# Performance work log

Hardware: AMD Instinct MI355X
Metric: run time of the kernel (lower is better)

## Reference

```python
import jax, jax.numpy as jnp
import numpy as np

DN = ('NCDHW', 'DHWIO', 'NCDHW')


def _w(key, cin, cout):
    # kernel_size=3 in 3D, Minkowski-style fan-in scaling, no bias
    scale = 1.0 / np.sqrt(cin * 27)
    return jax.random.normal(key, (3, 3, 3, cin, cout), dtype=jnp.float32) * scale


def setup_inputs() -> dict:
    key = jax.random.key(0)
    ks = jax.random.split(key, 7)
    x = jax.random.normal(ks[0], (1, 1024, 4, 4, 4), dtype=jnp.float32)
    chans = [(1024, 512), (512, 256), (256, 128), (128, 64), (64, 32), (32, 1)]
    ws = {f'w{i+1}': _w(ks[i + 1], ci, co) for i, (ci, co) in enumerate(chans)}
    return {'x': x, **ws}


def _ct(x, w, stride):
    # conv-transpose, kernel 3, SAME padding: stride 2 doubles resolution,
    # stride 1 preserves it (dense analog of Minkowski generative transpose conv)
    return jax.lax.conv_transpose(x, w, strides=(stride, stride, stride),
                                  padding='SAME', dimension_numbers=DN)


def reference(x, w1, w2, w3, w4, w5, w6):
    h = jax.nn.relu(_ct(x, w1, 2))   # 1024 -> 512, 4^3 -> 8^3
    h = jax.nn.relu(_ct(h, w2, 1))   # 512 -> 256
    h = jax.nn.relu(_ct(h, w3, 2))   # 256 -> 128, 8^3 -> 16^3
    h = jax.nn.relu(_ct(h, w4, 1))   # 128 -> 64
    h = jax.nn.relu(_ct(h, w5, 2))   # 64 -> 32, 16^3 -> 32^3
    return _ct(h, w6, 1)             # 32 -> 1, no final ReLU
```

## Files before the change

### kernel.cpp

```cpp
#include <hip/hip_runtime.h>

typedef _Float16 half8 __attribute__((ext_vector_type(8)));
typedef _Float16 half4v __attribute__((ext_vector_type(4)));
typedef float floatx4 __attribute__((ext_vector_type(4)));


__global__ __launch_bounds__(256) void pad_x_k(const float* __restrict__ X,
                                               _Float16* __restrict__ P) {
  int idx = blockIdx.x * 256 + threadIdx.x;
  if (idx >= 125 * 1024) return;
  int c = idx & 1023;
  int r = idx >> 10;
  int px = r % 5, py = (r / 5) % 5, pz = r / 25;
  float v = 0.f;
  if (px >= 1 && py >= 1 && pz >= 1)
    v = X[c * 64 + (pz - 1) * 16 + (py - 1) * 4 + (px - 1)];
  P[idx] = (_Float16)v;
}

template <int POS, int COUT, int S2IN, int NSPL, int PS>
__global__ __launch_bounds__(256) void red_k(const float* __restrict__ Pp,
                                             _Float16* __restrict__ P) {
  constexpr int C4 = COUT / 4;
  constexpr size_t U3 =
      S2IN ? (size_t)(POS / 2) * (POS / 2) * (POS / 2) : (size_t)POS * POS * POS;
  int idx = blockIdx.x * 256 + threadIdx.x;
  if (idx >= PS * PS * PS * C4) return;
  const int co = (idx % C4) * 4;
  const int r = idx / C4;
  const int px = r % PS, py = (r / PS) % PS, pz = r / (PS * PS);
  const int ix = px - 1, iy = py - 1, iz = pz - 1;
  float4 s = make_float4(0.f, 0.f, 0.f, 0.f);
  if ((unsigned)ix < (unsigned)POS && (unsigned)iy < (unsigned)POS &&
      (unsigned)iz < (unsigned)POS) {
    int j0, j1;
    size_t upos;
    if (S2IN) {
      const int pf[8] = {0, 8, 12, 16, 18, 22, 24, 26};
      const int tc[8] = {8, 4, 4, 2, 4, 2, 2, 1};
      const int cls = ((iz & 1) << 2) | ((iy & 1) << 1) | (ix & 1);
      j0 = pf[cls] * NSPL;
      j1 = j0 + tc[cls] * NSPL;
      constexpr int U = POS / 2;
      upos = ((size_t)(iz >> 1) * U + (iy >> 1)) * U + (ix >> 1);
    } else {
      j0 = 0;
      j1 = NSPL;
      upos = ((size_t)iz * POS + iy) * POS + ix;
    }
    const float* base = Pp + upos * COUT + co;
    for (int j = j0; j < j1; j++) {
      float4 v = *(const float4*)(base + (size_t)j * U3 * COUT);
      s.x += v.x; s.y += v.y; s.z += v.z; s.w += v.w;
    }
  }
  half4v h;
  h[0] = (_Float16)fmaxf(s.x, 0.f);
  h[1] = (_Float16)fmaxf(s.y, 0.f);
  h[2] = (_Float16)fmaxf(s.z, 0.f);
  h[3] = (_Float16)fmaxf(s.w, 0.f);
  *(half4v*)(P + (size_t)idx * 4) = h;
}

template <int CICHUNK, int CIN, int COUT, int NTILE, int TZ, int SOUTU,
          int PS, int SMODE, int TAPG, int STORE_MODE>
__global__ __launch_bounds__(256) void conv_mfma_k(
    const _Float16* __restrict__ P, const float* __restrict__ W,
    void* __restrict__ Optr) {
  constexpr int M = TZ * 16;
  constexpr bool S2 = (SMODE != 0);
  constexpr int MTZ = SOUTU / TZ;
  constexpr int MTXY = SOUTU / 4;
  constexpr int MT3 = MTZ * MTXY * MTXY;
  constexpr int KB = 32;
  constexpr int KP = 40;
  constexpr int KBI = CICHUNK / KB;
  constexpr int NCI = CIN / CICHUNK;
  constexpr int S = S2 ? 2 * SOUTU : SOUTU;
  constexpr int WM = (M == 128) ? 4 : 2;
  constexpr int NSUB = (WM == 4) ? (NTILE / 16) : (NTILE / 32);
  constexpr int BJ = KB * NTILE / 256;
  constexpr size_t U3 = (size_t)SOUTU * SOUTU * SOUTU;

  __shared__ __align__(16) _Float16 As[M][KP];
  __shared__ __align__(16) _Float16 Bs[NTILE][KP];

  int bx = blockIdx.x;
  int cls = 0, tap0 = 0, cig = blockIdx.z, jspl = 0;
  int p_toz = 0, p_toy = 0, p_tox = 0, p_wtap = 0;
  if (SMODE == 0) {
    const int tg = cig / NCI;
    cig -= tg * NCI;
    tap0 = tg * TAPG;
    jspl = blockIdx.z;
  } else if (SMODE == 1) {
    const int p = bx / MT3;
    bx -= p * MT3;
    jspl = p * NCI + cig;
    cls = (p >= 8) + (p >= 12) + (p >= 16) + (p >= 18) + (p >= 22) +
          (p >= 24) + (p >= 26);
    const int pf = cls == 0 ? 0 : cls == 1 ? 8 : cls == 2 ? 12
                 : cls == 3 ? 16 : cls == 4 ? 18 : cls == 5 ? 22
                 : cls == 6 ? 24 : 26;
    const int tl = p - pf;
    const int lz = (cls >> 2) & 1, ly = (cls >> 1) & 1, lx = cls & 1;
    const int shx = lx ? 0 : 1, shy = ly ? 0 : 1;
    const int iz = tl >> (shx + shy);
    const int rem = tl & ((1 << (shx + shy)) - 1);
    const int iy = rem >> shx;
    const int ix = rem & ((1 << shx) - 1);
    p_toz = lz ? 1 : iz;
    p_toy = ly ? 1 : iy;
    p_tox = lx ? 1 : ix;
    const int wz = lz ? 1 : 2 * iz, wy = ly ? 1 : 2 * iy,
              wx = lx ? 1 : 2 * ix;
    p_wtap = (wz * 3 + wy) * 3 + wx;
  } else {
    cls = bx / MT3;
    bx -= cls * MT3;
  }
  const int clz = (cls >> 2) & 1, cly = (cls >> 1) & 1, clx = cls & 1;

  const int u0z = (bx / (MTXY * MTXY)) * TZ;
  const int u0y = ((bx / MTXY) % MTXY) * 4;
  const int u0x = (bx % MTXY) * 4;
  const int n_base = blockIdx.y * NTILE;

  const int t = threadIdx.x;
  const int lane = t & 63;
  const int wave = t >> 6;

  const int skq = t & 3;
  const int sp = t >> 2;
  const int spx = sp & 3, spy = (sp >> 2) & 3, spz = sp >> 4;
  const int nB = t & (NTILE - 1);
  const int k0B = (t / NTILE) * BJ;
  const int m0w = (WM == 4) ? wave * 32 : (wave >> 1) * 32;
  const int n0w = (WM == 4) ? 0 : (wave & 1) * 32;
  const int fr = lane & 15;
  const int fq = lane >> 4;

  const int cz = S2 ? (clz ? 1 : 2) : 3;
  const int cy = S2 ? (cly ? 1 : 2) : 3;
  const int cx = S2 ? (clx ? 1 : 2) : 3;
  const int shx2 = clx ? 0 : 1, shy2 = cly ? 0 : 1;

  int NIT;
  if (SMODE == 0) NIT = TAPG * KBI;
  else if (SMODE == 1) NIT = KBI;
  else NIT = cz * cy * cx * KBI;

  floatx4 acc[2][NSUB];
#pragma unroll
  for (int i = 0; i < 2; i++)
#pragma unroll
    for (int s = 0; s < NSUB; s++) acc[i][s] = {0.f, 0.f, 0.f, 0.f};

  half8 rA0 = {}, rA1 = {}, nA0 = {}, nA1 = {};
  float rB[BJ] = {}, nBv[BJ] = {};

  auto load_it = [&](int it, half8& A0, half8& A1, float* BW) {
    int tap, kb;
    if (SMODE == 1) { tap = 0; kb = it; }
    else if (KBI == 1) { tap = it; kb = 0; }
    else { tap = it / KBI; kb = it - tap * KBI; }
    int toz, toy, tox, wtap;
    if (SMODE == 1) {
      toz = p_toz; toy = p_toy; tox = p_tox; wtap = p_wtap;
    } else if (SMODE == 0) {
      const int tt = tap0 + tap;
      const int iz = tt / 9;
      const int rem = tt - iz * 9;
      const int iy = rem / 3;
      const int ix = rem - iy * 3;
      toz = iz; toy = iy; tox = ix;
      wtap = tt;
    } else {
      const int iz = tap >> (shx2 + shy2);
      const int rem = tap & ((1 << (shx2 + shy2)) - 1);
      const int iy = rem >> shx2;
      const int ix = rem & ((1 << shx2) - 1);
      toz = clz ? 1 : iz; toy = cly ? 1 : iy; tox = clx ? 1 : ix;
      const int wz = clz ? 1 : 2 * iz, wy = cly ? 1 : 2 * iy,
                wx = clx ? 1 : 2 * ix;
      wtap = (wz * 3 + wy) * 3 + wx;
    }
    const int kof0 = cig * CICHUNK + kb * KB;
    const size_t pb =
        ((size_t)(((u0z + toz + spz) * PS + (u0y + toy + spy)) * PS +
                  (u0x + tox + spx))) * CIN + kof0 + skq * 8;
    A0 = *(const half8*)(P + pb);
    if (M == 128)
      A1 = *(const half8*)(P + pb + (size_t)4 * PS * PS * CIN);
    const float* wb =
        W + ((size_t)wtap * CIN + kof0 + k0B) * COUT + n_base + nB;
#pragma unroll
    for (int j = 0; j < BJ; j++) BW[j] = wb[(size_t)j * COUT];
  };

  load_it(0, rA0, rA1, rB);

  for (int it = 0; it < NIT; ++it) {
    *(half8*)&As[sp][skq * 8] = rA0;
    if (M == 128) *(half8*)&As[sp + 64][skq * 8] = rA1;
    if (BJ == 8) {
      half8 hb;
#pragma unroll
      for (int j = 0; j < 8; j++) hb[j] = (_Float16)rB[j];
      *(half8*)&Bs[nB][k0B] = hb;
    } else {
      half4v hb;
#pragma unroll
      for (int j = 0; j < 4; j++) hb[j] = (_Float16)rB[j];
      *(half4v*)&Bs[nB][k0B] = hb;
    }
    __syncthreads();
    if (it + 1 < NIT) load_it(it + 1, nA0, nA1, nBv);
    half8 a0 = *(const half8*)&As[m0w + fr][fq * 8];
    half8 a1 = *(const half8*)&As[m0w + 16 + fr][fq * 8];
#pragma unroll
    for (int s = 0; s < NSUB; s++) {
      half8 b = *(const half8*)&Bs[n0w + s * 16 + fr][fq * 8];
      acc[0][s] = __builtin_amdgcn_mfma_f32_16x16x32_f16(a0, b, acc[0][s], 0, 0, 0);
      acc[1][s] = __builtin_amdgcn_mfma_f32_16x16x32_f16(a1, b, acc[1][s], 0, 0, 0);
    }
    __syncthreads();
    rA0 = nA0;
    rA1 = nA1;
#pragma unroll
    for (int j = 0; j < BJ; j++) rB[j] = nBv[j];
  }

#pragma unroll
  for (int i = 0; i < 2; i++) {
#pragma unroll
    for (int r = 0; r < 4; r++) {
      const int m = m0w + i * 16 + fq * 4 + r;
      const int mz = m >> 4, my = (m >> 2) & 3, mx = m & 3;
      if (STORE_MODE == 2) {
        const int oz = 2 * (u0z + mz) + clz;
        const int oy = 2 * (u0y + my) + cly;
        const int ox = 2 * (u0x + mx) + clx;
        _Float16* o = (_Float16*)Optr +
            ((size_t)(((oz + 1) * (S + 2) + (oy + 1)) * (S + 2) + (ox + 1))) *
                COUT + n_base + n0w;
#pragma unroll
        for (int s = 0; s < NSUB; s++)
          o[s * 16 + fr] = (_Float16)fmaxf(acc[i][s][r], 0.f);
      } else {
        const size_t pos =
            ((size_t)((u0z + mz) * SOUTU + (u0y + my))) * SOUTU + (u0x + mx);
        float* o = (float*)Optr + ((size_t)jspl * U3 + pos) * COUT + n_base +
                   n0w;
#pragma unroll
        for (int s = 0; s < NSUB; s++) o[s * 16 + fr] = acc[i][s][r];
      }
    }
  }
}

__global__ __launch_bounds__(256) void conv6_k(const _Float16* __restrict__ P,
                                               const float* __restrict__ W6,
                                               float* __restrict__ O) {
  __shared__ __align__(16) float w[864];
  for (int i = threadIdx.x; i < 864; i += 256) w[i] = W6[i];
  __syncthreads();
  int idx = blockIdx.x * 256 + threadIdx.x;
  int x = idx & 31, y = (idx >> 5) & 31, z = idx >> 10;
  float a = 0.f;
  for (int dz = 0; dz < 3; dz++)
    for (int dy = 0; dy < 3; dy++)
      for (int dx = 0; dx < 3; dx++) {
        const _Float16* p =
            P + (size_t)(((z + dz) * 34 + (y + dy)) * 34 + (x + dx)) * 32;
        const float* ww = &w[((dz * 3 + dy) * 3 + dx) * 32];
#pragma unroll
        for (int c = 0; c < 32; c += 8) {
          half8 pv = *(const half8*)&p[c];
#pragma unroll
          for (int u = 0; u < 8; u++) a += (float)pv[u] * ww[c + u];
        }
      }
  O[idx] = a;
}

extern "C" void kernel_launch(void* const* d_in, const int* in_sizes, int n_in,
                              void* d_out, int out_size, void* d_ws,
                              size_t ws_size, hipStream_t stream) {
  const float* x  = (const float*)d_in[0];
  const float* w1 = (const float*)d_in[1];
  const float* w2 = (const float*)d_in[2];
  const float* w3 = (const float*)d_in[3];
  const float* w4 = (const float*)d_in[4];
  const float* w5 = (const float*)d_in[5];
  const float* w6 = (const float*)d_in[6];
  float* out = (float*)d_out;

  float* Q1 = (float*)d_ws;
  float* Q2 = Q1 + 3538944;
  float* Q3 = Q2 + 3145728;
  float* Q4 = Q3 + 3538944;
  _Float16* P1 = (_Float16*)(Q4 + 3145728);
  _Float16* P2 = P1 + 128000;
  _Float16* P3 = P2 + 512000;
  _Float16* P4 = P3 + 186624;
  _Float16* P5 = P4 + 746496;
  _Float16* P6 = P5 + 314432;

  hipMemsetAsync(P6, 0, 1257728 * sizeof(_Float16), stream);

  pad_x_k<<<500, 256, 0, stream>>>(x, P1);
  conv_mfma_k<256, 1024, 512, 64, 4, 4, 5, 1, 0, 3>
      <<<dim3(27, 8, 4), 256, 0, stream>>>(P1, w1, Q1);
  red_k<8, 512, 1, 4, 10><<<500, 256, 0, stream>>>(Q1, P2);
  conv_mfma_k<64, 512, 256, 64, 8, 8, 10, 0, 9, 3>
      <<<dim3(4, 4, 24), 256, 0, stream>>>(P2, w2, Q2);
  red_k<8, 256, 0, 24, 9><<<183, 256, 0, stream>>>(Q2, P3);
  conv_mfma_k<128, 256, 128, 64, 8, 8, 9, 1, 0, 3>
      <<<dim3(108, 2, 2), 256, 0, stream>>>(P3, w3, Q3);
  red_k<16, 128, 1, 2, 18><<<729, 256, 0, stream>>>(Q3, P4);
  conv_mfma_k<32, 128, 64, 64, 8, 16, 18, 0, 9, 3>
      <<<dim3(32, 1, 12), 256, 0, stream>>>(P4, w4, Q4);
  red_k<16, 64, 0, 12, 17><<<308, 256, 0, stream>>>(Q4, P5);
  conv_mfma_k<64, 64, 32, 32, 8, 16, 17, 2, 0, 2>
      <<<dim3(256, 1, 1), 256, 0, stream>>>(P5, w5, P6);
  conv6_k<<<128, 256, 0, stream>>>(P6, w6, out);

  (void)in_sizes; (void)n_in; (void)out_size; (void)ws_size;
}
```

Baseline: 208.5 us.

## Double-buffer LDS with two-deep register prefetch and wider K blocks

The MFMA conv kernel now uses two LDS buffers for A and B, with global loads prefetched two iterations ahead. Each iteration has a single barrier instead of two. The K block per iteration becomes a template parameter (64 for most layers), which halves the number of iterations and barriers. Layer 1 is split further over input-channel chunks (8-way instead of 4), so the partial-sum workspace and the reduce pass grow. The cost is roughly double the LDS and more registers, which may lower occupancy.

```diff
diff --git a/kernel.cpp b/kernel.cpp
--- a/kernel.cpp
+++ b/kernel.cpp
@@ -4,6 +4,10 @@
 typedef _Float16 half4v __attribute__((ext_vector_type(4)));
 typedef float floatx4 __attribute__((ext_vector_type(4)));
 
+
+__device__ __forceinline__ void sync_lds() {
+  asm volatile("s_waitcnt lgkmcnt(0)\n\ts_barrier" ::: "memory");
+}
 
 __global__ __launch_bounds__(256) void pad_x_k(const float* __restrict__ X,
                                                _Float16* __restrict__ P) {
@@ -63,7 +67,7 @@
 }
 
 template <int CICHUNK, int CIN, int COUT, int NTILE, int TZ, int SOUTU,
-          int PS, int SMODE, int TAPG, int STORE_MODE>
+          int PS, int SMODE, int TAPG, int STORE_MODE, int KB>
 __global__ __launch_bounds__(256) void conv_mfma_k(
     const _Float16* __restrict__ P, const float* __restrict__ W,
     void* __restrict__ Optr) {
@@ -72,18 +76,18 @@
   constexpr int MTZ = SOUTU / TZ;
   constexpr int MTXY = SOUTU / 4;
   constexpr int MT3 = MTZ * MTXY * MTXY;
-  constexpr int KB = 32;
-  constexpr int KP = 40;
+  constexpr int KP = KB + 8;
   constexpr int KBI = CICHUNK / KB;
   constexpr int NCI = CIN / CICHUNK;
   constexpr int S = S2 ? 2 * SOUTU : SOUTU;
   constexpr int WM = (M == 128) ? 4 : 2;
   constexpr int NSUB = (WM == 4) ? (NTILE / 16) : (NTILE / 32);
   constexpr int BJ = KB * NTILE / 256;
+  constexpr int AH = KB / 32;
   constexpr size_t U3 = (size_t)SOUTU * SOUTU * SOUTU;
 
-  __shared__ __align__(16) _Float16 As[M][KP];
-  __shared__ __align__(16) _Float16 Bs[NTILE][KP];
+  __shared__ __align__(16) _Float16 As[2][M][KP];
+  __shared__ __align__(16) _Float16 Bs[2][NTILE][KP];
 
   int bx = blockIdx.x;
   int cls = 0, tap0 = 0, cig = blockIdx.z, jspl = 0;
@@ -145,10 +149,8 @@
   const int cx = S2 ? (clx ? 1 : 2) : 3;
   const int shx2 = clx ? 0 : 1, shy2 = cly ? 0 : 1;
 
-  int NIT;
-  if (SMODE == 0) NIT = TAPG * KBI;
-  else if (SMODE == 1) NIT = KBI;
-  else NIT = cz * cy * cx * KBI;
+  const int NIT = (SMODE == 2) ? cz * cy * cx * KBI
+                               : (SMODE == 0 ? TAPG * KBI : KBI);
 
   floatx4 acc[2][NSUB];
 #pragma unroll
@@ -156,10 +158,14 @@
 #pragma unroll
     for (int s = 0; s < NSUB; s++) acc[i][s] = {0.f, 0.f, 0.f, 0.f};
 
-  half8 rA0 = {}, rA1 = {}, nA0 = {}, nA1 = {};
-  float rB[BJ] = {}, nBv[BJ] = {};
-
-  auto load_it = [&](int it, half8& A0, half8& A1, float* BW) {
+  struct RS {
+    half8 a0[AH];
+    half8 a1[AH];
+    float b[BJ];
+  };
+  RS s0, s1;
+
+  auto load_it = [&](int it, RS& R) {
     int tap, kb;
     if (SMODE == 1) { tap = 0; kb = it; }
     else if (KBI == 1) { tap = it; kb = 0; }
@@ -188,47 +194,65 @@
     const int kof0 = cig * CICHUNK + kb * KB;
     const size_t pb =
         ((size_t)(((u0z + toz + spz) * PS + (u0y + toy + spy)) * PS +
-                  (u0x + tox + spx))) * CIN + kof0 + skq * 8;
-    A0 = *(const half8*)(P + pb);
-    if (M == 128)
-      A1 = *(const half8*)(P + pb + (size_t)4 * PS * PS * CIN);
+                  (u0x + tox + spx))) * CIN + kof0 + skq * (8 * AH);
+#pragma unroll
+    for (int h = 0; h < AH; h++) R.a0[h] = *(const half8*)(P + pb + h * 8);
+    if (M == 128) {
+#pragma unroll
+      for (int h = 0; h < AH; h++)
+        R.a1[h] = *(const half8*)(P + pb + (size_t)4 * PS * PS * CIN + h * 8);
+    }
     const float* wb =
         W + ((size_t)wtap * CIN + kof0 + k0B) * COUT + n_base + nB;
 #pragma unroll
-    for (int j = 0; j < BJ; j++) BW[j] = wb[(size_t)j * COUT];
+    for (int j = 0; j < BJ; j++) R.b[j] = wb[(size_t)j * COUT];
   };
 
-  load_it(0, rA0, rA1, rB);
-
+  auto stage = [&](int buf, RS& R) {
+#pragma unroll
+    for (int h = 0; h < AH; h++)
+      *(half8*)&As[buf][sp][skq * 8 * AH + h * 8] = R.a0[h];
+    if (M == 128) {
+#pragma unroll
+      for (int h = 0; h < AH; h++)
+        *(half8*)&As[buf][sp + 64][skq * 8 * AH + h * 8] = R.a1[h];
+    }
+#pragma unroll
+    for (int g = 0; g < BJ / 8; g++) {
+      half8 hb;
+#pragma unroll
+      for (int j = 0; j < 8; j++) hb[j] = (_Float16)R.b[g * 8 + j];
+      *(half8*)&Bs[buf][nB][k0B + g * 8] = hb;
+    }
+  };
+
+  auto mfma_step = [&](int buf) {
+#pragma unroll
+    for (int ks = 0; ks < KB / 32; ks++) {
+      const int ko = ks * 32 + fq * 8;
+      half8 a0 = *(const half8*)&As[buf][m0w + fr][ko];
+      half8 a1 = *(const half8*)&As[buf][m0w + 16 + fr][ko];
+#pragma unroll
+      for (int s = 0; s < NSUB; s++) {
+        half8 b = *(const half8*)&Bs[buf][n0w + s * 16 + fr][ko];
+        acc[0][s] =
+            __builtin_amdgcn_mfma_f32_16x16x32_f16(a0, b, acc[0][s], 0, 0, 0);
+        acc[1][s] =
+            __builtin_amdgcn_mfma_f32_16x16x32_f16(a1, b, acc[1][s], 0, 0, 0);
+      }
+    }
+  };
+
+  load_it(0, s0);
+  if (NIT > 1) load_it(1, s1);
+  stage(0, s0);
+  sync_lds();
   for (int it = 0; it < NIT; ++it) {
-    *(half8*)&As[sp][skq * 8] = rA0;
-    if (M == 128) *(half8*)&As[sp + 64][skq * 8] = rA1;
-    if (BJ == 8) {
-      half8 hb;
-#pragma unroll
-      for (int j = 0; j < 8; j++) hb[j] = (_Float16)rB[j];
-      *(half8*)&Bs[nB][k0B] = hb;
-    } else {
-      half4v hb;
-#pragma unroll
-      for (int j = 0; j < 4; j++) hb[j] = (_Float16)rB[j];
-      *(half4v*)&Bs[nB][k0B] = hb;
-    }
-    __syncthreads();
-    if (it + 1 < NIT) load_it(it + 1, nA0, nA1, nBv);
-    half8 a0 = *(const half8*)&As[m0w + fr][fq * 8];
-    half8 a1 = *(const half8*)&As[m0w + 16 + fr][fq * 8];
-#pragma unroll
-    for (int s = 0; s < NSUB; s++) {
-      half8 b = *(const half8*)&Bs[n0w + s * 16 + fr][fq * 8];
-      acc[0][s] = __builtin_amdgcn_mfma_f32_16x16x32_f16(a0, b, acc[0][s], 0, 0, 0);
-      acc[1][s] = __builtin_amdgcn_mfma_f32_16x16x32_f16(a1, b, acc[1][s], 0, 0, 0);
-    }
-    __syncthreads();
-    rA0 = nA0;
-    rA1 = nA1;
-#pragma unroll
-    for (int j = 0; j < BJ; j++) rB[j] = nBv[j];
+    const int cb = it & 1;
+    if (it + 2 < NIT) load_it(it + 2, cb ? s1 : s0);
+    mfma_step(cb);
+    if (it + 1 < NIT) stage(cb ^ 1, cb ? s0 : s1);
+    sync_lds();
   }
 
 #pragma unroll
@@ -297,7 +321,7 @@
   float* out = (float*)d_out;
 
   float* Q1 = (float*)d_ws;
-  float* Q2 = Q1 + 3538944;
+  float* Q2 = Q1 + 7077888;
   float* Q3 = Q2 + 3145728;
   float* Q4 = Q3 + 3538944;
   _Float16* P1 = (_Float16*)(Q4 + 3145728);
@@ -310,19 +334,19 @@
   hipMemsetAsync(P6, 0, 1257728 * sizeof(_Float16), stream);
 
   pad_x_k<<<500, 256, 0, stream>>>(x, P1);
-  conv_mfma_k<256, 1024, 512, 64, 4, 4, 5, 1, 0, 3>
-      <<<dim3(27, 8, 4), 256, 0, stream>>>(P1, w1, Q1);
-  red_k<8, 512, 1, 4, 10><<<500, 256, 0, stream>>>(Q1, P2);
-  conv_mfma_k<64, 512, 256, 64, 8, 8, 10, 0, 9, 3>
+  conv_mfma_k<128, 1024, 512, 64, 4, 4, 5, 1, 0, 3, 64>
+      <<<dim3(27, 8, 8), 256, 0, stream>>>(P1, w1, Q1);
+  red_k<8, 512, 1, 8, 10><<<500, 256, 0, stream>>>(Q1, P2);
+  conv_mfma_k<64, 512, 256, 64, 8, 8, 10, 0, 9, 3, 64>
       <<<dim3(4, 4, 24), 256, 0, stream>>>(P2, w2, Q2);
   red_k<8, 256, 0, 24, 9><<<183, 256, 0, stream>>>(Q2, P3);
-  conv_mfma_k<128, 256, 128, 64, 8, 8, 9, 1, 0, 3>
+  conv_mfma_k<128, 256, 128, 64, 8, 8, 9, 1, 0, 3, 64>
       <<<dim3(108, 2, 2), 256, 0, stream>>>(P3, w3, Q3);
   red_k<16, 128, 1, 2, 18><<<729, 256, 0, stream>>>(Q3, P4);
-  conv_mfma_k<32, 128, 64, 64, 8, 16, 18, 0, 9, 3>
+  conv_mfma_k<32, 128, 64, 64, 8, 16, 18, 0, 9, 3, 32>
       <<<dim3(32, 1, 12), 256, 0, stream>>>(P4, w4, Q4);
   red_k<16, 64, 0, 12, 17><<<308, 256, 0, stream>>>(Q4, P5);
-  conv_mfma_k<64, 64, 32, 32, 8, 16, 17, 2, 0, 2>
+  conv_mfma_k<64, 64, 32, 32, 8, 16, 17, 2, 0, 2, 64>
       <<<dim3(256, 1, 1), 256, 0, stream>>>(P5, w5, P6);
   conv6_k<<<128, 256, 0, stream>>>(P6, w6, out);
 
```

After: 213.1 us. 2.2% more time.
